# Kernel tuning notes

Measured on AMD Instinct MI355X. Metric: run time of the kernel, lower is better.

## Reference

```python
import jax, jax.numpy as jnp
import numpy as np

B, N, D, H = 16, 512, 256, 8
DK = D // H
EPS = 1e-6
NEG_INF = 1e12
LAM_ATT, LAM_DIST, LAM_ADJ = 0.3, 0.3, 0.4


def setup_inputs() -> dict:
    key = jax.random.key(0)
    ks = jax.random.split(key, 16)
    inp = {
        "query": jax.random.normal(ks[0], (B, N, D), jnp.float32),
        "key": jax.random.normal(ks[1], (B, N, D), jnp.float32),
        "value": jax.random.normal(ks[2], (B, N, D), jnp.float32),
        "adj_matrix": jax.random.uniform(ks[3], (B, N, N), jnp.float32),
        "distances_matrix": jax.random.uniform(ks[4], (B, N, N), jnp.float32),
        "edges_att": jnp.zeros((1,), jnp.float32),
        "mask": jnp.ones((B, N), jnp.int32),
    }
    s = 1.0 / np.sqrt(D)
    # four Linear(d_model, d_model): Wq, Wk, Wv, Wo (+ biases)
    for i, nm in enumerate(["q", "k", "v", "o"]):
        inp[f"W{nm}"] = jax.random.normal(ks[5 + 2 * i], (D, D), jnp.float32) * s
        inp[f"b{nm}"] = jax.random.normal(ks[6 + 2 * i], (D,), jnp.float32) * s
    return inp


def _proj(x, W, b):
    # [B,N,D] -> [B,H,N,DK]
    y = x @ W.T + b
    return y.reshape(B, N, H, DK).transpose(0, 2, 1, 3)


def reference(query, key, value, adj_matrix, distances_matrix, edges_att, mask,
              Wq, bq, Wk, bk, Wv, bv, Wo, bo):
    q = _proj(query, Wq, bq)
    k = _proj(key, Wk, bk)
    v = _proj(value, Wv, bv)

    valid = mask != 0  # [B,N] key-side validity

    # distance kernel: softmax(-d) over keys, masked positions -> 0 prob
    d_scores = jnp.where(valid[:, None, :], -distances_matrix, -jnp.inf)
    p_dist = jax.nn.softmax(d_scores, axis=-1)  # [B,N,N]

    # scaled dot-product attention with key mask
    scores = jnp.einsum("bhqd,bhkd->bhqk", q, k) / np.sqrt(DK)
    scores = jnp.where(valid[:, None, None, :], scores, -NEG_INF)
    p_attn = jax.nn.softmax(scores, axis=-1)  # [B,H,N,N]

    # row-normalized adjacency
    p_adj = adj_matrix / (adj_matrix.sum(axis=-1, keepdims=True) + EPS)  # [B,N,N]

    # blend three attention terms (broadcast dist/adj over heads)
    p_weighted = (LAM_ATT * p_attn
                  + LAM_DIST * p_dist[:, None]
                  + LAM_ADJ * p_adj[:, None])  # [B,H,N,N]

    x = jnp.einsum("bhqk,bhkd->bhqd", p_weighted, v)  # [B,H,N,DK]
    x = x.transpose(0, 2, 1, 3).reshape(B, N, D)
    out = x @ Wo.T + bo  # output projection (4th linear)
    return out
```

## Files before the change

### kernel.cpp

```cpp
#include <hip/hip_runtime.h>
#include <cstdint>
#include <cstddef>

#define B_  16
#define N_  512
#define D_  256
#define H_  8
#define DK_ 32

#define QKV_ELEMS 2097152

__device__ __align__(16) unsigned short g_Qb[QKV_ELEMS];
__device__ __align__(16) unsigned short g_Kb[QKV_ELEMS];
__device__ __align__(16) unsigned short g_VT[QKV_ELEMS];
__device__ __align__(16) unsigned short g_WqB[D_*D_];
__device__ __align__(16) unsigned short g_WkB[D_*D_];
__device__ __align__(16) unsigned short g_WvB[D_*D_];
__device__ __align__(16) unsigned short g_WoB[D_*D_];
__device__ __align__(16) unsigned short g_ST[B_*N_*N_];

typedef short v8s __attribute__((ext_vector_type(8)));
typedef float v4f __attribute__((ext_vector_type(4)));

#define QSCALE 0.25503485917270874f

__device__ __forceinline__ unsigned short f2b(float f){
  unsigned int x;
  __builtin_memcpy(&x, &f, 4);
  x = x + 0x7FFFu + ((x >> 16) & 1u);
  return (unsigned short)(x >> 16);
}
__device__ __forceinline__ v8s pack8(const float4 a, const float4 b){
  v8s o;
  o[0]=(short)f2b(a.x); o[1]=(short)f2b(a.y); o[2]=(short)f2b(a.z); o[3]=(short)f2b(a.w);
  o[4]=(short)f2b(b.x); o[5]=(short)f2b(b.y); o[6]=(short)f2b(b.z); o[7]=(short)f2b(b.w);
  return o;
}

__global__ __launch_bounds__(256) void prep_w(
    const float* __restrict__ Wq, const float* __restrict__ Wk,
    const float* __restrict__ Wv, const float* __restrict__ Wo)
{
  const int bid = blockIdx.x;
  const int z = bid >> 6;
  const int i = ((bid & 63)*256 + (int)threadIdx.x)*4;
  const float* src = (z==0)?Wq:(z==1)?Wk:(z==2)?Wv:Wo;
  const float4 u = *reinterpret_cast<const float4*>(src + i);
  ushort4 o4;
  o4.x = f2b(u.x); o4.y = f2b(u.y); o4.z = f2b(u.z); o4.w = f2b(u.w);
  if (z < 3){
    unsigned short* dst = (z==0)?g_WqB:(z==1)?g_WkB:g_WvB;
    *reinterpret_cast<ushort4*>(dst + i) = o4;
  } else {
    const int n = i >> 8, k = i & 255;
    *reinterpret_cast<ushort4*>(g_WoB + ((size_t)(k >> 5))*8192 + (size_t)n*32 + (k & 31)) = o4;
  }
}

__global__ __launch_bounds__(256) void st_gemm(
    const float* __restrict__ query, const float* __restrict__ key_,
    const float* __restrict__ value,
    const float* __restrict__ bq, const float* __restrict__ bk,
    const float* __restrict__ bv,
    const float* __restrict__ dist, const float* __restrict__ adjm,
    const int* __restrict__ mask)
{
  __shared__ unsigned short Wl[64*264];
  const int bid0 = blockIdx.x;
  const int t    = threadIdx.x;

  if (bid0 >= 1536){
    const int s = bid0 - 1536;
    const int b = (s >> 1) & 15, qt = s >> 5, half = s & 1;
    const int row = half*8 + (t >> 5);
    const int seg = t & 31;
    const size_t roff = ((size_t)(b*N_ + qt*16 + row))*N_ + seg*16;
    const float* dp = dist + roff;
    const float* ap = adjm + roff;
    const int*   mp = mask + b*N_ + seg*16;
    const float4 d0 = reinterpret_cast<const float4*>(dp)[0];
    const float4 d1 = reinterpret_cast<const float4*>(dp)[1];
    const float4 d2 = reinterpret_cast<const float4*>(dp)[2];
    const float4 d3 = reinterpret_cast<const float4*>(dp)[3];
    const float4 a0 = reinterpret_cast<const float4*>(ap)[0];
    const float4 a1 = reinterpret_cast<const float4*>(ap)[1];
    const float4 a2 = reinterpret_cast<const float4*>(ap)[2];
    const float4 a3 = reinterpret_cast<const float4*>(ap)[3];
    const int4   m0 = reinterpret_cast<const int4*>(mp)[0];
    const int4   m1 = reinterpret_cast<const int4*>(mp)[1];
    const int4   m2 = reinterpret_cast<const int4*>(mp)[2];
    const int4   m3 = reinterpret_cast<const int4*>(mp)[3];

    float ev[16], av[16];
    #define ST_STEP(i, d4, a4, m4) \
      ev[i+0] = m4.x ? __expf(-d4.x) : 0.f;  av[i+0] = a4.x; \
      ev[i+1] = m4.y ? __expf(-d4.y) : 0.f;  av[i+1] = a4.y; \
      ev[i+2] = m4.z ? __expf(-d4.z) : 0.f;  av[i+2] = a4.z; \
      ev[i+3] = m4.w ? __expf(-d4.w) : 0.f;  av[i+3] = a4.w;
    ST_STEP(0,  d0, a0, m0)
    ST_STEP(4,  d1, a1, m1)
    ST_STEP(8,  d2, a2, m2)
    ST_STEP(12, d3, a3, m3)
    #undef ST_STEP
    float lz = 0.f, la = 0.f;
    #pragma unroll
    for (int i = 0; i < 16; ++i){ lz += ev[i]; la += av[i]; }
    #pragma unroll
    for (int o = 1; o < 32; o <<= 1){
      lz += __shfl_xor(lz, o, 64);
      la += __shfl_xor(la, o, 64);
    }
    const float c0 = (lz > 0.f) ? 0.3f / lz : 0.f;
    const float c1 = 0.4f / (la + 1e-6f);
    v8s s0v, s1v;
    #pragma unroll
    for (int i = 0; i < 8; ++i){
      s0v[i] = (short)f2b(ev[i]*c0   + av[i]*c1);
      s1v[i] = (short)f2b(ev[8+i]*c0 + av[8+i]*c1);
    }
    *reinterpret_cast<v8s*>(g_ST + roff)     = s0v;
    *reinterpret_cast<v8s*>(g_ST + roff + 8) = s1v;
    return;
  }

  const int bid = ((bid0 & 7) * 192) + (bid0 >> 3);
  const int z  = bid >> 9;
  const int rr = bid & 511;
  const int mt = rr >> 2, nt = rr & 3;
  const float* Ap = (z==0) ? query : (z==1) ? key_ : value;
  const unsigned short* WB = (z==0) ? g_WqB : (z==1) ? g_WkB : g_WvB;
  const float* bp = (z==0) ? bq : (z==1) ? bk : bv;
  const int w = t >> 6, lane = t & 63, kl = lane & 15, quad = lane >> 4;
  const int m0 = mt*64 + w*16;
  const int n0 = nt*64;

  {
    const int row = t >> 2;
    const int ks  = (t & 3) * 64;
    const unsigned short* src = WB + (size_t)(n0+row)*256 + ks;
    unsigned short* dst = Wl + row*264 + ks;
    #pragma unroll
    for (int u = 0; u < 8; ++u)
      *reinterpret_cast<v8s*>(dst + u*8) = *reinterpret_cast<const v8s*>(src + u*8);
  }
  __syncthreads();

  v4f acc[4];
  #pragma unroll
  for (int nb = 0; nb < 4; ++nb) acc[nb] = (v4f){0.f,0.f,0.f,0.f};
  const int arow = m0 + kl;

  if (z == 2){
    #pragma unroll
    for (int k0 = 0; k0 < 256; k0 += 32){
      const float* ap = Ap + (size_t)arow*256 + k0 + quad*8;
      const v8s af = pack8(reinterpret_cast<const float4*>(ap)[0],
                           reinterpret_cast<const float4*>(ap)[1]);
      #pragma unroll
      for (int nb = 0; nb < 4; ++nb){
        const v8s wf = *reinterpret_cast<const v8s*>(&Wl[(nb*16+kl)*264 + k0 + quad*8]);
        acc[nb] = __builtin_amdgcn_mfma_f32_16x16x32_bf16(wf, af, acc[nb], 0, 0, 0);
      }
    }
    const int tok = m0 + kl, bb = tok >> 9, nr = tok & 511;
    #pragma unroll
    for (int nb = 0; nb < 4; ++nb)
      #pragma unroll
      for (int r = 0; r < 4; ++r){
        const int n = n0 + nb*16 + quad*4 + r;
        const float v = acc[nb][r] + bp[n];
        g_VT[(((size_t)bb*H_ + (n>>5))*16 + (nr>>5))*1024 + (size_t)(n&31)*32 + (nr&31)] = f2b(v);
      }
  } else {
    #pragma unroll
    for (int k0 = 0; k0 < 256; k0 += 32){
      const float* ap = Ap + (size_t)arow*256 + k0 + quad*8;
      const v8s af = pack8(reinterpret_cast<const float4*>(ap)[0],
                           reinterpret_cast<const float4*>(ap)[1]);
      #pragma unroll
      for (int nb = 0; nb < 4; ++nb){
        const v8s wf = *reinterpret_cast<const v8s*>(&Wl[(nb*16+kl)*264 + k0 + quad*8]);
        acc[nb] = __builtin_amdgcn_mfma_f32_16x16x32_bf16(af, wf, acc[nb], 0, 0, 0);
      }
    }
    unsigned short* dst = z ? g_Kb : g_Qb;
    const float sc = (z == 0) ? QSCALE : 1.0f;
    #pragma unroll
    for (int nb = 0; nb < 4; ++nb){
      const int n = n0 + nb*16 + kl;
      const float bias = bp[n];
      #pragma unroll
      for (int r = 0; r < 4; ++r){
        const int m = m0 + quad*4 + r;
        const float v = (acc[nb][r] + bias) * sc;
        dst[(((size_t)(m>>9)*H_ + (n>>5))*N_ + (m&511))*DK_ + (n&31)] = f2b(v);
      }
    }
  }
}

__global__ __launch_bounds__(512, 4) void attn_kernel(
    const int* __restrict__ mask, const float* __restrict__ bo,
    float* __restrict__ out)
{
  __shared__ unsigned short STl[16*520];
  __shared__ unsigned short Xl[16*272];
  const int bid = blockIdx.x;
  const int b  = bid & 15;
  const int qt = bid >> 4;
  const int q0 = qt*16;
  const int t  = threadIdx.x;
  const int w  = t >> 6, lane = t & 63;
  const int kl = lane & 15, quad = lane >> 4;

  {
    const int row = t >> 5;
    const int c16 = (t & 31) * 16;
    const unsigned short* src = g_ST + ((size_t)(b*N_ + q0 + row))*N_ + c16;
    *reinterpret_cast<v8s*>(&STl[row*520 + c16])     = *reinterpret_cast<const v8s*>(src);
    *reinterpret_cast<v8s*>(&STl[row*520 + c16 + 8]) = *reinterpret_cast<const v8s*>(src + 8);
  }

  const int h = w;
  const size_t bh = (size_t)b*H_ + h;
  const unsigned short* Qp = g_Qb + (bh*N_ + q0)*DK_;
  const unsigned short* Kp = g_Kb + bh*N_*DK_;
  const unsigned short* Vp = g_VT + bh*(size_t)(N_*DK_);
  const int* mrow = mask + b*N_;
  const v8s aq = *reinterpret_cast<const v8s*>(Qp + (size_t)kl*DK_ + quad*8);
  const v4f vz = {0.f, 0.f, 0.f, 0.f};

  const int s0 = ((quad & 1) << 5) + kl;
  const int s1 = s0 + 16;
  const int hi = quad >> 1;

  v4f oA0 = vz, oA1 = vz;
  v4f oS0 = vz, oS1 = vz;
  float lsum = 0.f;

  __syncthreads();

  #pragma unroll 1
  for (int ch = 0; ch < 4; ++ch){
    const int k0 = ch*128;
    v4f acc[8];
    #pragma unroll
    for (int kb = 0; kb < 8; ++kb){
      const v8s bk = *reinterpret_cast<const v8s*>(Kp + (size_t)(k0 + kb*16 + kl)*DK_ + quad*8);
      acc[kb] = __builtin_amdgcn_mfma_f32_16x16x32_bf16(bk, aq, vz, 0, 0, 0);
    }
    v8s av[8];
    #pragma unroll
    for (int cc = 0; cc < 4; ++cc){
      const int kk = k0 + cc*32;
      av[2*cc]   = *reinterpret_cast<const v8s*>(Vp + (size_t)(kk + kl)*32 + quad*8);
      av[2*cc+1] = *reinterpret_cast<const v8s*>(Vp + (size_t)(kk + 16 + kl)*32 + quad*8);
    }
    #pragma unroll
    for (int kb = 0; kb < 8; ++kb){
      const int4 m4 = *reinterpret_cast<const int4*>(mrow + k0 + kb*16 + quad*4);
      const float e0 = m4.x ? __builtin_amdgcn_exp2f(acc[kb][0]) : 0.f;
      const float e1 = m4.y ? __builtin_amdgcn_exp2f(acc[kb][1]) : 0.f;
      const float e2 = m4.z ? __builtin_amdgcn_exp2f(acc[kb][2]) : 0.f;
      const float e3 = m4.w ? __builtin_amdgcn_exp2f(acc[kb][3]) : 0.f;
      acc[kb][0]=e0; acc[kb][1]=e1; acc[kb][2]=e2; acc[kb][3]=e3;
      lsum += e0+e1+e2+e3;
    }
    #pragma unroll
    for (int cc = 0; cc < 4; ++cc){
      const int kk = k0 + cc*32;
      uint32_t pkE0, pkE2, pkO0, pkO2;
      asm("v_cvt_pk_bf16_f32 %0, %1, %2" : "=v"(pkE0) : "v"(acc[2*cc][0]),   "v"(acc[2*cc][1]));
      asm("v_cvt_pk_bf16_f32 %0, %1, %2" : "=v"(pkE2) : "v"(acc[2*cc][2]),   "v"(acc[2*cc][3]));
      asm("v_cvt_pk_bf16_f32 %0, %1, %2" : "=v"(pkO0) : "v"(acc[2*cc+1][0]), "v"(acc[2*cc+1][1]));
      asm("v_cvt_pk_bf16_f32 %0, %1, %2" : "=v"(pkO2) : "v"(acc[2*cc+1][2]), "v"(acc[2*cc+1][3]));
      const uint32_t e0a = (uint32_t)__shfl((int)pkE0, s0, 64);
      const uint32_t o0a = (uint32_t)__shfl((int)pkO0, s0, 64);
      const uint32_t e2a = (uint32_t)__shfl((int)pkE2, s0, 64);
      const uint32_t o2a = (uint32_t)__shfl((int)pkO2, s0, 64);
      const uint32_t e0b = (uint32_t)__shfl((int)pkE0, s1, 64);
      const uint32_t o0b = (uint32_t)__shfl((int)pkO0, s1, 64);
      const uint32_t e2b = (uint32_t)__shfl((int)pkE2, s1, 64);
      const uint32_t o2b = (uint32_t)__shfl((int)pkO2, s1, 64);
      union { v8s v; uint32_t w4[4]; } bp;
      bp.w4[0] = hi ? o0a : e0a;
      bp.w4[1] = hi ? o2a : e2a;
      bp.w4[2] = hi ? o0b : e0b;
      bp.w4[3] = hi ? o2b : e2b;
      const v8s bst = *reinterpret_cast<const v8s*>(&STl[kl*520 + kk + quad*8]);
      oA0 = __builtin_amdgcn_mfma_f32_16x16x32_bf16(av[2*cc],   bp.v, oA0, 0, 0, 0);
      oS0 = __builtin_amdgcn_mfma_f32_16x16x32_bf16(av[2*cc],   bst,  oS0, 0, 0, 0);
      oA1 = __builtin_amdgcn_mfma_f32_16x16x32_bf16(av[2*cc+1], bp.v, oA1, 0, 0, 0);
      oS1 = __builtin_amdgcn_mfma_f32_16x16x32_bf16(av[2*cc+1], bst,  oS1, 0, 0, 0);
    }
  }

  lsum += __shfl_xor(lsum, 16, 64);
  lsum += __shfl_xor(lsum, 32, 64);
  const float inv = (lsum > 0.f) ? 0.3f / lsum : 0.f;

  unsigned short* xr = Xl + kl*272 + h*32;
  #pragma unroll
  for (int r = 0; r < 4; ++r){
    xr[     quad*4 + r] = f2b(oA0[r]*inv + oS0[r]);
    xr[16 + quad*4 + r] = f2b(oA1[r]*inv + oS1[r]);
  }
  __syncthreads();

  {
    const int n0 = w*32;
    v4f a2[2];
    a2[0] = vz; a2[1] = vz;
    #pragma unroll
    for (int k0 = 0; k0 < 256; k0 += 32){
      const v8s af = *reinterpret_cast<const v8s*>(&Xl[kl*272 + k0 + quad*8]);
      #pragma unroll
      for (int nb = 0; nb < 2; ++nb){
        const v8s wf = *reinterpret_cast<const v8s*>(
            g_WoB + (size_t)(k0 >> 5)*8192 + (size_t)(n0 + nb*16 + kl)*32 + quad*8);
        a2[nb] = __builtin_amdgcn_mfma_f32_16x16x32_bf16(af, wf, a2[nb], 0, 0, 0);
      }
    }
    #pragma unroll
    for (int nb = 0; nb < 2; ++nb){
      const int n = n0 + nb*16 + kl;
      const float bias = bo[n];
      #pragma unroll
      for (int r = 0; r < 4; ++r)
        out[((size_t)(b*N_ + q0 + quad*4 + r))*256 + n] = a2[nb][r] + bias;
    }
  }
}

extern "C" void kernel_launch(void* const* d_in, const int* in_sizes, int n_in,
                              void* d_out, int out_size, void* d_ws, size_t ws_size,
                              hipStream_t stream)
{
  const float* query = (const float*)d_in[0];
  const float* key_  = (const float*)d_in[1];
  const float* value = (const float*)d_in[2];
  const float* adjm  = (const float*)d_in[3];
  const float* dist  = (const float*)d_in[4];
  const int*   mask  = (const int*)d_in[6];
  const float* Wq = (const float*)d_in[7];  const float* bq = (const float*)d_in[8];
  const float* Wk = (const float*)d_in[9];  const float* bk = (const float*)d_in[10];
  const float* Wv = (const float*)d_in[11]; const float* bv = (const float*)d_in[12];
  const float* Wo = (const float*)d_in[13]; const float* bo = (const float*)d_in[14];

  prep_w<<<256, 256, 0, stream>>>(Wq, Wk, Wv, Wo);
  st_gemm<<<2560, 256, 0, stream>>>(query, key_, value, bq, bk, bv,
                                    dist, adjm, mask);
  attn_kernel<<<512, 512, 0, stream>>>(mask, bo, (float*)d_out);
}
```

Before: 164.2 us.

## Pre-convert QKV activations to bf16 in prep kernel and split QKV GEMM

```diff
diff --git a/kernel.cpp b/kernel.cpp
--- a/kernel.cpp
+++ b/kernel.cpp
@@ -13,6 +13,7 @@
 __device__ __align__(16) unsigned short g_Qb[QKV_ELEMS];
 __device__ __align__(16) unsigned short g_Kb[QKV_ELEMS];
 __device__ __align__(16) unsigned short g_VT[QKV_ELEMS];
+__device__ __align__(16) unsigned short g_Ain[3*QKV_ELEMS];
 __device__ __align__(16) unsigned short g_WqB[D_*D_];
 __device__ __align__(16) unsigned short g_WkB[D_*D_];
 __device__ __align__(16) unsigned short g_WvB[D_*D_];
@@ -37,40 +38,19 @@
   return o;
 }
 
-__global__ __launch_bounds__(256) void prep_w(
+__global__ __launch_bounds__(256) void prep(
+    const float* __restrict__ dist, const float* __restrict__ adjm,
+    const int* __restrict__ mask,
+    const float* __restrict__ query, const float* __restrict__ key_,
+    const float* __restrict__ value,
     const float* __restrict__ Wq, const float* __restrict__ Wk,
     const float* __restrict__ Wv, const float* __restrict__ Wo)
 {
   const int bid = blockIdx.x;
-  const int z = bid >> 6;
-  const int i = ((bid & 63)*256 + (int)threadIdx.x)*4;
-  const float* src = (z==0)?Wq:(z==1)?Wk:(z==2)?Wv:Wo;
-  const float4 u = *reinterpret_cast<const float4*>(src + i);
-  ushort4 o4;
-  o4.x = f2b(u.x); o4.y = f2b(u.y); o4.z = f2b(u.z); o4.w = f2b(u.w);
-  if (z < 3){
-    unsigned short* dst = (z==0)?g_WqB:(z==1)?g_WkB:g_WvB;
-    *reinterpret_cast<ushort4*>(dst + i) = o4;
-  } else {
-    const int n = i >> 8, k = i & 255;
-    *reinterpret_cast<ushort4*>(g_WoB + ((size_t)(k >> 5))*8192 + (size_t)n*32 + (k & 31)) = o4;
-  }
-}
-
-__global__ __launch_bounds__(256) void st_gemm(
-    const float* __restrict__ query, const float* __restrict__ key_,
-    const float* __restrict__ value,
-    const float* __restrict__ bq, const float* __restrict__ bk,
-    const float* __restrict__ bv,
-    const float* __restrict__ dist, const float* __restrict__ adjm,
-    const int* __restrict__ mask)
-{
-  __shared__ unsigned short Wl[64*264];
-  const int bid0 = blockIdx.x;
-  const int t    = threadIdx.x;
-
-  if (bid0 >= 1536){
-    const int s = bid0 - 1536;
+  const int t   = threadIdx.x;
+
+  if (bid < 1024){
+    const int s = bid;
     const int b = (s >> 1) & 15, qt = s >> 5, half = s & 1;
     const int row = half*8 + (t >> 5);
     const int seg = t & 31;
@@ -123,11 +103,50 @@
     return;
   }
 
+  if (bid < 2560){
+    const int a = bid - 1024;
+    const int z = a >> 9;
+    const int blk = a & 511;
+    const size_t base = ((size_t)blk*256 + t) * 16;
+    const float* src = (z==0)?query:(z==1)?key_:value;
+    const float4 u0 = reinterpret_cast<const float4*>(src + base)[0];
+    const float4 u1 = reinterpret_cast<const float4*>(src + base)[1];
+    const float4 u2 = reinterpret_cast<const float4*>(src + base)[2];
+    const float4 u3 = reinterpret_cast<const float4*>(src + base)[3];
+    unsigned short* dst = g_Ain + (size_t)z*QKV_ELEMS + base;
+    *reinterpret_cast<v8s*>(dst)     = pack8(u0, u1);
+    *reinterpret_cast<v8s*>(dst + 8) = pack8(u2, u3);
+    return;
+  }
+
+  const int wb = bid - 2560;
+  const int z = wb >> 6;
+  const int i = ((wb & 63)*256 + t)*4;
+  const float* src = (z==0)?Wq:(z==1)?Wk:(z==2)?Wv:Wo;
+  const float4 u = *reinterpret_cast<const float4*>(src + i);
+  ushort4 o4;
+  o4.x = f2b(u.x); o4.y = f2b(u.y); o4.z = f2b(u.z); o4.w = f2b(u.w);
+  if (z < 3){
+    unsigned short* dst = (z==0)?g_WqB:(z==1)?g_WkB:g_WvB;
+    *reinterpret_cast<ushort4*>(dst + i) = o4;
+  } else {
+    const int n = i >> 8, k = i & 255;
+    *reinterpret_cast<ushort4*>(g_WoB + ((size_t)(k >> 5))*8192 + (size_t)n*32 + (k & 31)) = o4;
+  }
+}
+
+__global__ __launch_bounds__(256) void qkv_gemm(
+    const float* __restrict__ bq, const float* __restrict__ bk,
+    const float* __restrict__ bv)
+{
+  __shared__ unsigned short Wl[64*264];
+  const int bid0 = blockIdx.x;
+  const int t    = threadIdx.x;
   const int bid = ((bid0 & 7) * 192) + (bid0 >> 3);
   const int z  = bid >> 9;
   const int rr = bid & 511;
   const int mt = rr >> 2, nt = rr & 3;
-  const float* Ap = (z==0) ? query : (z==1) ? key_ : value;
+  const unsigned short* Ap = g_Ain + (size_t)z*QKV_ELEMS;
   const unsigned short* WB = (z==0) ? g_WqB : (z==1) ? g_WkB : g_WvB;
   const float* bp = (z==0) ? bq : (z==1) ? bk : bv;
   const int w = t >> 6, lane = t & 63, kl = lane & 15, quad = lane >> 4;
@@ -153,9 +172,7 @@
   if (z == 2){
     #pragma unroll
     for (int k0 = 0; k0 < 256; k0 += 32){
-      const float* ap = Ap + (size_t)arow*256 + k0 + quad*8;
-      const v8s af = pack8(reinterpret_cast<const float4*>(ap)[0],
-                           reinterpret_cast<const float4*>(ap)[1]);
+      const v8s af = *reinterpret_cast<const v8s*>(Ap + (size_t)arow*256 + k0 + quad*8);
       #pragma unroll
       for (int nb = 0; nb < 4; ++nb){
         const v8s wf = *reinterpret_cast<const v8s*>(&Wl[(nb*16+kl)*264 + k0 + quad*8]);
@@ -174,9 +191,7 @@
   } else {
     #pragma unroll
     for (int k0 = 0; k0 < 256; k0 += 32){
-      const float* ap = Ap + (size_t)arow*256 + k0 + quad*8;
-      const v8s af = pack8(reinterpret_cast<const float4*>(ap)[0],
-                           reinterpret_cast<const float4*>(ap)[1]);
+      const v8s af = *reinterpret_cast<const v8s*>(Ap + (size_t)arow*256 + k0 + quad*8);
       #pragma unroll
       for (int nb = 0; nb < 4; ++nb){
         const v8s wf = *reinterpret_cast<const v8s*>(&Wl[(nb*16+kl)*264 + k0 + quad*8]);
@@ -347,8 +362,8 @@
   const float* Wv = (const float*)d_in[11]; const float* bv = (const float*)d_in[12];
   const float* Wo = (const float*)d_in[13]; const float* bo = (const float*)d_in[14];
 
-  prep_w<<<256, 256, 0, stream>>>(Wq, Wk, Wv, Wo);
-  st_gemm<<<2560, 256, 0, stream>>>(query, key_, value, bq, bk, bv,
-                                    dist, adjm, mask);
+  prep<<<2816, 256, 0, stream>>>(dist, adjm, mask, query, key_, value,
+                                 Wq, Wk, Wv, Wo);
+  qkv_gemm<<<1536, 256, 0, stream>>>(bq, bk, bv);
   attn_kernel<<<512, 512, 0, stream>>>(mask, bo, (float*)d_out);
 }
```

Measured after the change: 161.4 us (median of 2 runs). About the same (-1.7%).
